# Kernel tuning notes

Measured on AMD Instinct MI355X. Metric: run time of the kernel, lower is better.

## Reference

```python
import jax, jax.numpy as jnp
import numpy as np

N = 50000      # nodes
E = 1600000    # edges (avg degree 32)
F_IN = 128     # num_features
DIM = 64       # hidden dim
L = 3          # num_gc_layers
G = 500        # graphs in batch


def setup_inputs() -> dict:
    key = jax.random.key(0)
    ks = jax.random.split(key, 16)
    inp = {}
    inp["x"] = jax.random.normal(ks[0], (N, F_IN), dtype=jnp.float32)
    inp["edge_index"] = jax.random.randint(ks[1], (2, E), 0, N, dtype=jnp.int32)
    inp["batch"] = jnp.sort(jax.random.randint(ks[2], (N,), 0, G, dtype=jnp.int32))
    # GIN layer MLP params: layer0 maps F_IN->DIM->DIM, later layers DIM->DIM->DIM
    d_in = F_IN
    ki = 3
    for i in range(L):
        inp[f"W1_{i}"] = jax.random.normal(ks[ki], (d_in, DIM), dtype=jnp.float32) / np.sqrt(d_in); ki += 1
        inp[f"b1_{i}"] = jnp.zeros((DIM,), dtype=jnp.float32)
        inp[f"W2_{i}"] = jax.random.normal(ks[ki], (DIM, DIM), dtype=jnp.float32) / np.sqrt(DIM); ki += 1
        inp[f"b2_{i}"] = jnp.zeros((DIM,), dtype=jnp.float32)
        d_in = DIM
    # final scoring head: concat readout -> dim * L inputs, 1 output
    inp["Wm"] = jax.random.normal(ks[ki], (DIM * L, 1), dtype=jnp.float32) / np.sqrt(DIM * L)
    inp["bm"] = jnp.zeros((1,), dtype=jnp.float32)
    return inp


def _segment_softmax(scores, seg, num_segments):
    # numerically stable softmax over elements grouped by seg; scores [M, 1]
    m = jax.ops.segment_max(scores, seg, num_segments=num_segments)
    e = jnp.exp(scores - m[seg])
    denom = jax.ops.segment_sum(e, seg, num_segments=num_segments)
    return e / denom[seg]


def _forward(x, edge_index, batch, params):
    src, dst = edge_index[0], edge_index[1]
    n = x.shape[0]
    xs = []
    h = x
    for i in range(L):
        W1, b1, W2, b2 = params[4 * i: 4 * i + 4]
        # GINConv (eps=0): h_i <- MLP(h_i + sum_{j->i} h_j)
        agg = jax.ops.segment_sum(h[src], dst, num_segments=n)
        h = jax.nn.relu((h + agg) @ W1 + b1) @ W2 + b2
        if i != L - 1:
            h = jax.nn.relu(h)
        xs.append(h)
    node_prob = jnp.concatenate(xs, axis=1)            # concat readout [N, DIM*L]
    Wm, bm = params[4 * L], params[4 * L + 1]
    node_score = node_prob @ Wm + bm                   # [N, 1]
    # lift_node_score_to_edge_score
    src_score = node_score[src]                        # [E, 1]
    dst_score = node_score[dst]
    edge_score = src_score * dst_score
    edge_prop = _segment_softmax(edge_score, dst, n)   # softmax over edges per dst
    new_score = jax.ops.segment_sum(src_score * edge_prop, dst, num_segments=n)
    node_score = node_score + new_score
    # final softmax over nodes grouped by graph id
    return _segment_softmax(node_score, batch, G)


def reference(x, edge_index, batch, W1_0, b1_0, W2_0, b2_0, W1_1, b1_1, W2_1, b2_1,
              W1_2, b1_2, W2_2, b2_2, Wm, bm):
    params = [W1_0, b1_0, W2_0, b2_0, W1_1, b1_1, W2_1, b2_1,
              W1_2, b1_2, W2_2, b2_2, Wm, bm]
    return _forward(x, edge_index, batch, params)
```

## Files before the change

### kernel.cpp

```cpp
#include <hip/hip_runtime.h>
#include <hip/hip_fp16.h>
#include <math.h>

#define N_NODES 50000
#define N_EDGES 1600000
#define N_GRAPH 500
#define CHUNKS 128
#define EPC (N_EDGES / CHUNKS)
#define NP1 (N_NODES + 1)
#define NIT ((EPC + 1023) / 1024)
#define GEMM_BLOCKS 128

__device__ __forceinline__ float rl(float v, int k) {
    return __int_as_float(__builtin_amdgcn_readlane(__float_as_int(v), k));
}
__device__ __forceinline__ void hacc16(float4& A, float4& B, uint4 w) {
    float2 f0 = __half22float2(*reinterpret_cast<__half2*>(&w.x));
    float2 f1 = __half22float2(*reinterpret_cast<__half2*>(&w.y));
    float2 f2 = __half22float2(*reinterpret_cast<__half2*>(&w.z));
    float2 f3 = __half22float2(*reinterpret_cast<__half2*>(&w.w));
    A.x += f0.x; A.y += f0.y; A.z += f1.x; A.w += f1.y;
    B.x += f2.x; B.y += f2.y; B.z += f3.x; B.w += f3.y;
}

__global__ __launch_bounds__(1024) void hist_gemm0_kernel(const int* __restrict__ src,
                                                          const int* __restrict__ dst,
                                                          int* __restrict__ csrc_chunk,
                                                          unsigned short* __restrict__ locs,
                                                          const float* __restrict__ x,
                                                          const float* __restrict__ W1,
                                                          __half* __restrict__ y0, int N) {
    __shared__ unsigned packed[N_NODES / 2];
    __shared__ unsigned aux[1024];
    const int tid = threadIdx.x;

    if (blockIdx.x < CHUNKS) {
        const int c = blockIdx.x;
        const int s0 = c * EPC;

        for (int i = tid; i < N_NODES / 2; i += 1024) packed[i] = 0;
        __syncthreads();

        unsigned short lrv[NIT];
#pragma unroll
        for (int it = 0; it < NIT; it++) {
            int e = s0 + it * 1024 + tid;
            if (e < s0 + EPC) {
                int d = dst[e];
                int sh = (d & 1) * 16;
                unsigned old = atomicAdd(&packed[d >> 1], 1u << sh);
                lrv[it] = (unsigned short)((old >> sh) & 0xffffu);
            }
        }
        __syncthreads();

        const int W = 25;
        int w0 = tid * W;
        int w1 = min(w0 + W, N_NODES / 2);
        unsigned run = 0;
        for (int i = w0; i < w1; i++) {
            unsigned v = packed[i];
            unsigned lo = v & 0xffffu, hi = v >> 16;
            packed[i] = run | ((run + lo) << 16);
            run += lo + hi;
        }
        aux[tid] = run;
        __syncthreads();
        for (int off = 1; off < 1024; off <<= 1) {
            unsigned t = (tid >= off) ? aux[tid - off] : 0;
            __syncthreads();
            aux[tid] += t;
            __syncthreads();
        }
        unsigned b0 = (tid == 0) ? 0 : aux[tid - 1];
        if (b0) {
            unsigned addv = b0 | (b0 << 16);
            for (int i = w0; i < w1; i++) packed[i] += addv;
        }
        __syncthreads();

        int* outc = csrc_chunk + (size_t)c * EPC;
#pragma unroll
        for (int it = 0; it < NIT; it++) {
            int e = s0 + it * 1024 + tid;
            if (e < s0 + EPC) {
                int d = dst[e];
                unsigned pw = packed[d >> 1];
                unsigned loc = (d & 1) ? (pw >> 16) : (pw & 0xffffu);
                outc[loc + lrv[it]] = src[e];
            }
        }
        unsigned short* lc = locs + (size_t)c * NP1;
        for (int d = tid; d <= N_NODES; d += 1024) {
            unsigned short loc;
            if (d == N_NODES) {
                loc = (unsigned short)EPC;
            } else {
                unsigned pw = packed[d >> 1];
                loc = (unsigned short)((d & 1) ? (pw >> 16) : (pw & 0xffffu));
            }
            lc[d] = loc;
        }
    } else {
        float* sW = (float*)packed;
        for (int i = tid; i < 64 * 64; i += 1024) sW[i] = W1[64 * 64 + i];
        __syncthreads();
        int lane = tid & 63;
        float w[64];
#pragma unroll
        for (int k = 0; k < 64; k++) w[k] = W1[k * 64 + lane];
        int wid = ((blockIdx.x - CHUNKS) * 1024 + tid) >> 6;
        const int totalWaves = GEMM_BLOCKS * 16;
        for (int node = wid; node < N; node += totalWaves) {
            float xa = x[(size_t)node * 128 + lane];
            float xb = x[(size_t)node * 128 + 64 + lane];
            float a0 = 0.f, a1 = 0.f, a2 = 0.f, a3 = 0.f;
#pragma unroll
            for (int k = 0; k < 64; k += 4) {
                a0 = fmaf(rl(xa, k + 0), w[k + 0], a0);
                a1 = fmaf(rl(xa, k + 1), w[k + 1], a1);
                a2 = fmaf(rl(xa, k + 2), w[k + 2], a2);
                a3 = fmaf(rl(xa, k + 3), w[k + 3], a3);
            }
#pragma unroll
            for (int k = 0; k < 64; k += 4) {
                a0 = fmaf(rl(xb, k + 0), sW[(k + 0) * 64 + lane], a0);
                a1 = fmaf(rl(xb, k + 1), sW[(k + 1) * 64 + lane], a1);
                a2 = fmaf(rl(xb, k + 2), sW[(k + 2) * 64 + lane], a2);
                a3 = fmaf(rl(xb, k + 3), sW[(k + 3) * 64 + lane], a3);
            }
            y0[(size_t)node * 64 + lane] = __float2half((a0 + a1) + (a2 + a3));
        }
    }
}

__global__ __launch_bounds__(1024) void base_scan1_kernel(const unsigned short* __restrict__ locs,
                                                          unsigned short* __restrict__ base,
                                                          int* __restrict__ deg,
                                                          int* __restrict__ part, int N) {
    int d = blockIdx.x * 1024 + threadIdx.x;
    int run = 0;
    if (d < N) {
#pragma unroll 8
        for (int c = 0; c < CHUNKS; c++) {
            int l0 = locs[(size_t)c * NP1 + d];
            int l1 = locs[(size_t)c * NP1 + d + 1];
            base[(size_t)c * N + d] = (unsigned short)run;
            run += l1 - l0;
        }
        deg[d] = run;
    }
    int v = run;
#pragma unroll
    for (int o = 32; o >= 1; o >>= 1) v += __shfl_xor(v, o);
    __shared__ int red[16];
    if ((threadIdx.x & 63) == 0) red[threadIdx.x >> 6] = v;
    __syncthreads();
    if (threadIdx.x == 0) {
        int s = 0;
#pragma unroll
        for (int k = 0; k < 16; k++) s += red[k];
        part[blockIdx.x] = s;
    }
}

__global__ void scan2_kernel(int* __restrict__ part, int nb) {
    int lane = threadIdx.x;
    int v = (lane < nb) ? part[lane] : 0;
    int orig = v;
#pragma unroll
    for (int o = 1; o < 64; o <<= 1) {
        int t = __shfl_up(v, o);
        if (lane >= o) v += t;
    }
    if (lane < nb) part[lane] = v - orig;
    if (lane == nb - 1) part[nb] = v;
}

__global__ __launch_bounds__(1024) void scan3_kernel(const int* __restrict__ deg,
                                                     const int* __restrict__ part,
                                                     int* __restrict__ rowptr, int N) {
    int i = blockIdx.x * 1024 + threadIdx.x;
    int lane = threadIdx.x & 63;
    int w = threadIdx.x >> 6;
    int v = (i < N) ? deg[i] : 0;
    int inc = v;
#pragma unroll
    for (int o = 1; o < 64; o <<= 1) {
        int t = __shfl_up(inc, o);
        if (lane >= o) inc += t;
    }
    __shared__ int wsum[16];
    if (lane == 63) wsum[w] = inc;
    __syncthreads();
    if (threadIdx.x < 16) {
        int x = wsum[threadIdx.x];
        int xo = x;
#pragma unroll
        for (int o = 1; o < 16; o <<= 1) {
            int t = __shfl_up(x, o);
            if ((int)threadIdx.x >= o) x += t;
        }
        wsum[threadIdx.x] = x - xo;
    }
    __syncthreads();
    int b = part[blockIdx.x] + wsum[w];
    if (i < N) {
        rowptr[i] = b + inc - v;
        if (i == N - 1) rowptr[N] = b + inc;
    }
}

__global__ __launch_bounds__(256) void gatherfill_kernel(const int* __restrict__ csrc_chunk,
                                                         const unsigned short* __restrict__ locs,
                                                         const unsigned short* __restrict__ base,
                                                         const int* __restrict__ rowptr,
                                                         int* __restrict__ csr_src) {
    const int perXcd = N_NODES / 8;
    int xcd = blockIdx.x & 7;
    int idx = (blockIdx.x >> 3) * 4 + (threadIdx.x >> 6);
    if (idx >= perXcd) return;
    int wid = xcd * perXcd + idx;
    int lane = threadIdx.x & 63;
    int rp = rowptr[wid];
#pragma unroll
    for (int cc = 0; cc < 2; cc++) {
        int c = lane + cc * 64;
        const unsigned short* lc = locs + (size_t)c * NP1;
        int l0 = lc[wid];
        int l1 = lc[wid + 1];
        int cnt = l1 - l0;
        int ob = rp + (int)base[(size_t)c * N_NODES + wid];
        const int* in = csrc_chunk + (size_t)c * EPC + l0;
        for (int i = 0; i < cnt; i++) csr_src[ob + i] = in[i];
    }
}

__global__ __launch_bounds__(256) void agg_kernel(const __half* __restrict__ yh,
                                                  const int* __restrict__ rowptr,
                                                  const int* __restrict__ csr_src,
                                                  float* __restrict__ u, int N) {
    int wid = (blockIdx.x * 256 + threadIdx.x) >> 6;
    int lane = threadIdx.x & 63;
    if (wid >= N) return;
    int q = lane >> 3;
    int r = lane & 7;
    int start = rowptr[wid];
    int end = rowptr[wid + 1];
    float4 A = make_float4(0.f, 0.f, 0.f, 0.f);
    float4 B = make_float4(0.f, 0.f, 0.f, 0.f);
    int j = start;
    for (; j + 64 <= end; j += 64) {
        int s0 = csr_src[j + q];
        int s1 = csr_src[j + 8 + q];
        int s2 = csr_src[j + 16 + q];
        int s3 = csr_src[j + 24 + q];
        int s4 = csr_src[j + 32 + q];
        int s5 = csr_src[j + 40 + q];
        int s6 = csr_src[j + 48 + q];
        int s7 = csr_src[j + 56 + q];
        uint4 w0 = *(const uint4*)(yh + (size_t)s0 * 64 + r * 8);
        uint4 w1 = *(const uint4*)(yh + (size_t)s1 * 64 + r * 8);
        uint4 w2 = *(const uint4*)(yh + (size_t)s2 * 64 + r * 8);
        uint4 w3 = *(const uint4*)(yh + (size_t)s3 * 64 + r * 8);
        uint4 w4 = *(const uint4*)(yh + (size_t)s4 * 64 + r * 8);
        uint4 w5 = *(const uint4*)(yh + (size_t)s5 * 64 + r * 8);
        uint4 w6 = *(const uint4*)(yh + (size_t)s6 * 64 + r * 8);
        uint4 w7 = *(const uint4*)(yh + (size_t)s7 * 64 + r * 8);
        hacc16(A, B, w0); hacc16(A, B, w1); hacc16(A, B, w2); hacc16(A, B, w3);
        hacc16(A, B, w4); hacc16(A, B, w5); hacc16(A, B, w6); hacc16(A, B, w7);
    }
#pragma unroll
    for (int m = 0; m < 8; m++) {
        int e = j + 8 * m + q;
        if (e < end) {
            int s = csr_src[e];
            uint4 w = *(const uint4*)(yh + (size_t)s * 64 + r * 8);
            hacc16(A, B, w);
        }
    }
#pragma unroll
    for (int o = 8; o <= 32; o <<= 1) {
        A.x += __shfl_xor(A.x, o); A.y += __shfl_xor(A.y, o);
        A.z += __shfl_xor(A.z, o); A.w += __shfl_xor(A.w, o);
        B.x += __shfl_xor(B.x, o); B.y += __shfl_xor(B.y, o);
        B.z += __shfl_xor(B.z, o); B.w += __shfl_xor(B.w, o);
    }
    if (lane < 8) {
        uint4 w = *(const uint4*)(yh + (size_t)wid * 64 + r * 8);
        hacc16(A, B, w);
        *(float4*)(u + (size_t)wid * 64 + r * 8) = A;
        *(float4*)(u + (size_t)wid * 64 + r * 8 + 4) = B;
    }
}

template <int LAYER>
__global__ __launch_bounds__(256) void mlpAB_kernel(const float* __restrict__ u,
                                                    const float* __restrict__ b1,
                                                    const float* __restrict__ W2,
                                                    const float* __restrict__ b2,
                                                    const float* __restrict__ W1n,
                                                    const float* __restrict__ Wm,
                                                    __half* __restrict__ ynext,
                                                    float* __restrict__ score,
                                                    int N, int totalWaves) {
    int lane = threadIdx.x & 63;
    int wid = (blockIdx.x * 256 + threadIdx.x) >> 6;
    float w2[64], w1[64];
#pragma unroll
    for (int k = 0; k < 64; k++) w2[k] = W2[k * 64 + lane];
#pragma unroll
    for (int k = 0; k < 64; k++) w1[k] = W1n[k * 64 + lane];
    float bb1 = b1[lane], bb2 = b2[lane], wm = Wm[LAYER * 64 + lane];

    int node = wid;
    float uin = (node < N) ? u[(size_t)node * 64 + lane] : 0.f;
    for (; node < N; node += totalWaves) {
        int nn = node + totalWaves;
        float unext = (nn < N) ? u[(size_t)nn * 64 + lane] : 0.f;
        float t = fmaxf(uin + bb1, 0.f);
        float a0 = 0.f, a1 = 0.f, a2 = 0.f, a3 = 0.f;
#pragma unroll
        for (int k = 0; k < 64; k += 4) {
            a0 = fmaf(rl(t, k + 0), w2[k + 0], a0);
            a1 = fmaf(rl(t, k + 1), w2[k + 1], a1);
            a2 = fmaf(rl(t, k + 2), w2[k + 2], a2);
            a3 = fmaf(rl(t, k + 3), w2[k + 3], a3);
        }
        float h = fmaxf(bb2 + ((a0 + a1) + (a2 + a3)), 0.f);
        float p = h * wm;
#pragma unroll
        for (int o = 32; o >= 1; o >>= 1) p += __shfl_xor(p, o);
        if (lane == 0) {
            if (LAYER == 0) score[node] = p;
            else score[node] += p;
        }
        float y0 = 0.f, y1 = 0.f, y2 = 0.f, y3 = 0.f;
#pragma unroll
        for (int k = 0; k < 64; k += 4) {
            y0 = fmaf(rl(h, k + 0), w1[k + 0], y0);
            y1 = fmaf(rl(h, k + 1), w1[k + 1], y1);
            y2 = fmaf(rl(h, k + 2), w1[k + 2], y2);
            y3 = fmaf(rl(h, k + 3), w1[k + 3], y3);
        }
        ynext[(size_t)node * 64 + lane] = __float2half((y0 + y1) + (y2 + y3));
        uin = unext;
    }
}

__global__ __launch_bounds__(256) void mlpA2_kernel(const float* __restrict__ u,
                                                    const float* __restrict__ b1,
                                                    const float* __restrict__ W2,
                                                    const float* __restrict__ b2,
                                                    const float* __restrict__ Wm,
                                                    float* __restrict__ score,
                                                    int N, int totalWaves) {
    int lane = threadIdx.x & 63;
    int wid = (blockIdx.x * 256 + threadIdx.x) >> 6;
    float w2[64];
#pragma unroll
    for (int k = 0; k < 64; k++) w2[k] = W2[k * 64 + lane];
    float bb1 = b1[lane], bb2 = b2[lane], wm = Wm[2 * 64 + lane];

    int node = wid;
    float uin = (node < N) ? u[(size_t)node * 64 + lane] : 0.f;
    for (; node < N; node += totalWaves) {
        int nn = node + totalWaves;
        float unext = (nn < N) ? u[(size_t)nn * 64 + lane] : 0.f;
        float t = fmaxf(uin + bb1, 0.f);
        float a0 = 0.f, a1 = 0.f, a2 = 0.f, a3 = 0.f;
#pragma unroll
        for (int k = 0; k < 64; k += 4) {
            a0 = fmaf(rl(t, k + 0), w2[k + 0], a0);
            a1 = fmaf(rl(t, k + 1), w2[k + 1], a1);
            a2 = fmaf(rl(t, k + 2), w2[k + 2], a2);
            a3 = fmaf(rl(t, k + 3), w2[k + 3], a3);
        }
        float h = bb2 + ((a0 + a1) + (a2 + a3));
        float p = h * wm;
#pragma unroll
        for (int o = 32; o >= 1; o >>= 1) p += __shfl_xor(p, o);
        if (lane == 0) score[node] += p;
        uin = unext;
    }
}

__global__ __launch_bounds__(256) void edge_softmax_kernel(const float* __restrict__ score,
                                                           const int* __restrict__ rowptr,
                                                           const int* __restrict__ csr_src,
                                                           const float* __restrict__ bm,
                                                           float* __restrict__ nsf, int N) {
    int wid = (blockIdx.x * blockDim.x + threadIdx.x) >> 6;
    int lane = threadIdx.x & 63;
    if (wid >= N) return;
    float b = bm[0];
    float sd = score[wid] + b;
    int start = rowptr[wid];
    int end = rowptr[wid + 1];
    bool has0 = (start + lane < end);
    float ss0 = 0.f;
    float m = -INFINITY;
    if (has0) {
        ss0 = score[csr_src[start + lane]] + b;
        m = ss0 * sd;
    }
    for (int j = start + 64 + lane; j < end; j += 64) {
        float ss = score[csr_src[j]] + b;
        m = fmaxf(m, ss * sd);
    }
#pragma unroll
    for (int o = 32; o >= 1; o >>= 1) m = fmaxf(m, __shfl_xor(m, o));
    float se = 0.f, swe = 0.f;
    if (m > -INFINITY) {
        if (has0) {
            float e0 = expf(ss0 * sd - m);
            se += e0;
            swe += ss0 * e0;
        }
        for (int j = start + 64 + lane; j < end; j += 64) {
            float ss = score[csr_src[j]] + b;
            float e = expf(ss * sd - m);
            se += e;
            swe += ss * e;
        }
#pragma unroll
        for (int o = 32; o >= 1; o >>= 1) {
            se += __shfl_xor(se, o);
            swe += __shfl_xor(swe, o);
        }
    }
    float ns = (se > 0.f) ? (swe / se) : 0.f;
    if (lane == 0) nsf[wid] = sd + ns;
}

__global__ __launch_bounds__(256) void graph_softmax_kernel(const float* __restrict__ nsf,
                                                            const int* __restrict__ batch,
                                                            float* __restrict__ out, int N) {
    int g = blockIdx.x;
    int tid = threadIdx.x;
    int lo = 0, hi = N;
    while (lo < hi) { int mid = (lo + hi) >> 1; if (batch[mid] < g) lo = mid + 1; else hi = mid; }
    int s0 = lo;
    hi = N;
    while (lo < hi) { int mid = (lo + hi) >> 1; if (batch[mid] < g + 1) lo = mid + 1; else hi = mid; }
    int s1 = lo;

    __shared__ float red[4];
    __shared__ float bval;
    float m = -INFINITY;
    for (int i = s0 + tid; i < s1; i += 256) m = fmaxf(m, nsf[i]);
#pragma unroll
    for (int o = 32; o >= 1; o >>= 1) m = fmaxf(m, __shfl_xor(m, o));
    if ((tid & 63) == 0) red[tid >> 6] = m;
    __syncthreads();
    if (tid == 0) bval = fmaxf(fmaxf(red[0], red[1]), fmaxf(red[2], red[3]));
    __syncthreads();
    float bmx = bval;
    float s = 0.f;
    for (int i = s0 + tid; i < s1; i += 256) {
        float e = expf(nsf[i] - bmx);
        out[i] = e;
        s += e;
    }
#pragma unroll
    for (int o = 32; o >= 1; o >>= 1) s += __shfl_xor(s, o);
    __syncthreads();
    if ((tid & 63) == 0) red[tid >> 6] = s;
    __syncthreads();
    if (tid == 0) bval = red[0] + red[1] + red[2] + red[3];
    __syncthreads();
    float inv = 1.f / bval;
    for (int i = s0 + tid; i < s1; i += 256) out[i] *= inv;
}

extern "C" void kernel_launch(void* const* d_in, const int* in_sizes, int n_in,
                              void* d_out, int out_size, void* d_ws, size_t ws_size,
                              hipStream_t stream) {
    const int N = N_NODES, E = N_EDGES;

    const float* x = (const float*)d_in[0];
    const int* ei = (const int*)d_in[1];
    const int* batch = (const int*)d_in[2];
    const float* W1a[3] = {(const float*)d_in[3], (const float*)d_in[7], (const float*)d_in[11]};
    const float* b1a[3] = {(const float*)d_in[4], (const float*)d_in[8], (const float*)d_in[12]};
    const float* W2a[3] = {(const float*)d_in[5], (const float*)d_in[9], (const float*)d_in[13]};
    const float* b2a[3] = {(const float*)d_in[6], (const float*)d_in[10], (const float*)d_in[14]};
    const float* Wm = (const float*)d_in[15];
    const float* bm = (const float*)d_in[16];
    float* out = (float*)d_out;

    const int* srcp = ei;
    const int* dstp = ei + E;

    float* ubuf = (float*)d_ws;
    int* csrc_chunk = (int*)ubuf;
    __half* yA = (__half*)(ubuf + (size_t)N * 64);
    __half* yB = yA + (size_t)N * 64;
    float* score = (float*)(yB + (size_t)N * 64);
    float* nsf = score + N;
    int* deg = (int*)(nsf + N);
    int* rowptr = deg + N;
    int* part = rowptr + N + 1;
    int* csr_src = part + 64;
    unsigned short* locs = (unsigned short*)(csr_src + E);
    unsigned short* base = locs + (size_t)CHUNKS * NP1;

    hist_gemm0_kernel<<<CHUNKS + GEMM_BLOCKS, 1024, 0, stream>>>(srcp, dstp, csrc_chunk, locs,
                                                                 x, W1a[0], yA, N);

    const int nbScan = (N + 1023) / 1024;
    base_scan1_kernel<<<nbScan, 1024, 0, stream>>>(locs, base, deg, part, N);
    scan2_kernel<<<1, 64, 0, stream>>>(part, nbScan);
    scan3_kernel<<<nbScan, 1024, 0, stream>>>(deg, part, rowptr, N);

    const int gfBlocks = 8 * ((N / 8 + 3) / 4);
    gatherfill_kernel<<<gfBlocks, 256, 0, stream>>>(csrc_chunk, locs, base, rowptr, csr_src);

    const int gw = 4096;
    int aggBlocks = (N + 3) / 4;

    agg_kernel<<<aggBlocks, 256, 0, stream>>>(yA, rowptr, csr_src, ubuf, N);
    mlpAB_kernel<0><<<1024, 256, 0, stream>>>(ubuf, b1a[0], W2a[0], b2a[0], W1a[1], Wm, yB, score, N, gw);

    agg_kernel<<<aggBlocks, 256, 0, stream>>>(yB, rowptr, csr_src, ubuf, N);
    mlpAB_kernel<1><<<1024, 256, 0, stream>>>(ubuf, b1a[1], W2a[1], b2a[1], W1a[2], Wm, yA, score, N, gw);

    agg_kernel<<<aggBlocks, 256, 0, stream>>>(yA, rowptr, csr_src, ubuf, N);
    mlpA2_kernel<<<1024, 256, 0, stream>>>(ubuf, b1a[2], W2a[2], b2a[2], Wm, score, N, gw);

    edge_softmax_kernel<<<(N + 3) / 4, 256, 0, stream>>>(score, rowptr, csr_src, bm, nsf, N);

    graph_softmax_kernel<<<N_GRAPH, 256, 0, stream>>>(nsf, batch, out, N);
}
```

Baseline: 372.5 us.

## Move layer-0 GEMM into gather-fill kernel and fold scan2 into scan3

The first-layer x@W1 GEMM moves out of the histogram-sort kernel and is co-launched with the CSR gather-fill kernel as extra 256-thread blocks, so it no longer competes with the LDS-heavy sort blocks. The GEMM now keeps the weights in registers and does two passes over the two 64-wide halves of x, writing and then rereading the half-precision output. This adds a second fp16 rounding and an extra read-modify-write of y0. The separate scan2 launch is removed: each scan3 block reduces the per-block partial sums itself, which saves one kernel launch.

```diff
diff --git a/kernel.cpp b/kernel.cpp
--- a/kernel.cpp
+++ b/kernel.cpp
@@ -9,7 +9,7 @@
 #define EPC (N_EDGES / CHUNKS)
 #define NP1 (N_NODES + 1)
 #define NIT ((EPC + 1023) / 1024)
-#define GEMM_BLOCKS 128
+#define GEMM_BLOCKS 1024
 
 __device__ __forceinline__ float rl(float v, int k) {
     return __int_as_float(__builtin_amdgcn_readlane(__float_as_int(v), k));
@@ -23,114 +23,78 @@
     B.x += f2.x; B.y += f2.y; B.z += f3.x; B.w += f3.y;
 }
 
-__global__ __launch_bounds__(1024) void hist_gemm0_kernel(const int* __restrict__ src,
-                                                          const int* __restrict__ dst,
-                                                          int* __restrict__ csrc_chunk,
-                                                          unsigned short* __restrict__ locs,
-                                                          const float* __restrict__ x,
-                                                          const float* __restrict__ W1,
-                                                          __half* __restrict__ y0, int N) {
+__global__ __launch_bounds__(1024) void histsort_kernel(const int* __restrict__ src,
+                                                        const int* __restrict__ dst,
+                                                        int* __restrict__ csrc_chunk,
+                                                        unsigned short* __restrict__ locs) {
     __shared__ unsigned packed[N_NODES / 2];
     __shared__ unsigned aux[1024];
+    const int c = blockIdx.x;
+    const int s0 = c * EPC;
     const int tid = threadIdx.x;
 
-    if (blockIdx.x < CHUNKS) {
-        const int c = blockIdx.x;
-        const int s0 = c * EPC;
-
-        for (int i = tid; i < N_NODES / 2; i += 1024) packed[i] = 0;
+    for (int i = tid; i < N_NODES / 2; i += 1024) packed[i] = 0;
+    __syncthreads();
+
+    unsigned short lrv[NIT];
+#pragma unroll
+    for (int it = 0; it < NIT; it++) {
+        int e = s0 + it * 1024 + tid;
+        if (e < s0 + EPC) {
+            int d = dst[e];
+            int sh = (d & 1) * 16;
+            unsigned old = atomicAdd(&packed[d >> 1], 1u << sh);
+            lrv[it] = (unsigned short)((old >> sh) & 0xffffu);
+        }
+    }
+    __syncthreads();
+
+    const int W = 25;
+    int w0 = tid * W;
+    int w1 = min(w0 + W, N_NODES / 2);
+    unsigned run = 0;
+    for (int i = w0; i < w1; i++) {
+        unsigned v = packed[i];
+        unsigned lo = v & 0xffffu, hi = v >> 16;
+        packed[i] = run | ((run + lo) << 16);
+        run += lo + hi;
+    }
+    aux[tid] = run;
+    __syncthreads();
+    for (int off = 1; off < 1024; off <<= 1) {
+        unsigned t = (tid >= off) ? aux[tid - off] : 0;
         __syncthreads();
-
-        unsigned short lrv[NIT];
-#pragma unroll
-        for (int it = 0; it < NIT; it++) {
-            int e = s0 + it * 1024 + tid;
-            if (e < s0 + EPC) {
-                int d = dst[e];
-                int sh = (d & 1) * 16;
-                unsigned old = atomicAdd(&packed[d >> 1], 1u << sh);
-                lrv[it] = (unsigned short)((old >> sh) & 0xffffu);
-            }
-        }
+        aux[tid] += t;
         __syncthreads();
-
-        const int W = 25;
-        int w0 = tid * W;
-        int w1 = min(w0 + W, N_NODES / 2);
-        unsigned run = 0;
-        for (int i = w0; i < w1; i++) {
-            unsigned v = packed[i];
-            unsigned lo = v & 0xffffu, hi = v >> 16;
-            packed[i] = run | ((run + lo) << 16);
-            run += lo + hi;
-        }
-        aux[tid] = run;
-        __syncthreads();
-        for (int off = 1; off < 1024; off <<= 1) {
-            unsigned t = (tid >= off) ? aux[tid - off] : 0;
-            __syncthreads();
-            aux[tid] += t;
-            __syncthreads();
-        }
-        unsigned b0 = (tid == 0) ? 0 : aux[tid - 1];
-        if (b0) {
-            unsigned addv = b0 | (b0 << 16);
-            for (int i = w0; i < w1; i++) packed[i] += addv;
-        }
-        __syncthreads();
-
-        int* outc = csrc_chunk + (size_t)c * EPC;
-#pragma unroll
-        for (int it = 0; it < NIT; it++) {
-            int e = s0 + it * 1024 + tid;
-            if (e < s0 + EPC) {
-                int d = dst[e];
-                unsigned pw = packed[d >> 1];
-                unsigned loc = (d & 1) ? (pw >> 16) : (pw & 0xffffu);
-                outc[loc + lrv[it]] = src[e];
-            }
-        }
-        unsigned short* lc = locs + (size_t)c * NP1;
-        for (int d = tid; d <= N_NODES; d += 1024) {
-            unsigned short loc;
-            if (d == N_NODES) {
-                loc = (unsigned short)EPC;
-            } else {
-                unsigned pw = packed[d >> 1];
-                loc = (unsigned short)((d & 1) ? (pw >> 16) : (pw & 0xffffu));
-            }
-            lc[d] = loc;
-        }
-    } else {
-        float* sW = (float*)packed;
-        for (int i = tid; i < 64 * 64; i += 1024) sW[i] = W1[64 * 64 + i];
-        __syncthreads();
-        int lane = tid & 63;
-        float w[64];
-#pragma unroll
-        for (int k = 0; k < 64; k++) w[k] = W1[k * 64 + lane];
-        int wid = ((blockIdx.x - CHUNKS) * 1024 + tid) >> 6;
-        const int totalWaves = GEMM_BLOCKS * 16;
-        for (int node = wid; node < N; node += totalWaves) {
-            float xa = x[(size_t)node * 128 + lane];
-            float xb = x[(size_t)node * 128 + 64 + lane];
-            float a0 = 0.f, a1 = 0.f, a2 = 0.f, a3 = 0.f;
-#pragma unroll
-            for (int k = 0; k < 64; k += 4) {
-                a0 = fmaf(rl(xa, k + 0), w[k + 0], a0);
-                a1 = fmaf(rl(xa, k + 1), w[k + 1], a1);
-                a2 = fmaf(rl(xa, k + 2), w[k + 2], a2);
-                a3 = fmaf(rl(xa, k + 3), w[k + 3], a3);
-            }
-#pragma unroll
-            for (int k = 0; k < 64; k += 4) {
-                a0 = fmaf(rl(xb, k + 0), sW[(k + 0) * 64 + lane], a0);
-                a1 = fmaf(rl(xb, k + 1), sW[(k + 1) * 64 + lane], a1);
-                a2 = fmaf(rl(xb, k + 2), sW[(k + 2) * 64 + lane], a2);
-                a3 = fmaf(rl(xb, k + 3), sW[(k + 3) * 64 + lane], a3);
-            }
-            y0[(size_t)node * 64 + lane] = __float2half((a0 + a1) + (a2 + a3));
-        }
+    }
+    unsigned b0 = (tid == 0) ? 0 : aux[tid - 1];
+    if (b0) {
+        unsigned addv = b0 | (b0 << 16);
+        for (int i = w0; i < w1; i++) packed[i] += addv;
+    }
+    __syncthreads();
+
+    int* outc = csrc_chunk + (size_t)c * EPC;
+#pragma unroll
+    for (int it = 0; it < NIT; it++) {
+        int e = s0 + it * 1024 + tid;
+        if (e < s0 + EPC) {
+            int d = dst[e];
+            unsigned pw = packed[d >> 1];
+            unsigned loc = (d & 1) ? (pw >> 16) : (pw & 0xffffu);
+            outc[loc + lrv[it]] = src[e];
+        }
+    }
+    unsigned short* lc = locs + (size_t)c * NP1;
+    for (int d = tid; d <= N_NODES; d += 1024) {
+        unsigned short loc;
+        if (d == N_NODES) {
+            loc = (unsigned short)EPC;
+        } else {
+            unsigned pw = packed[d >> 1];
+            loc = (unsigned short)((d & 1) ? (pw >> 16) : (pw & 0xffffu));
+        }
+        lc[d] = loc;
     }
 }
 
@@ -164,25 +128,20 @@
     }
 }
 
-__global__ void scan2_kernel(int* __restrict__ part, int nb) {
-    int lane = threadIdx.x;
-    int v = (lane < nb) ? part[lane] : 0;
-    int orig = v;
-#pragma unroll
-    for (int o = 1; o < 64; o <<= 1) {
-        int t = __shfl_up(v, o);
-        if (lane >= o) v += t;
-    }
-    if (lane < nb) part[lane] = v - orig;
-    if (lane == nb - 1) part[nb] = v;
-}
-
 __global__ __launch_bounds__(1024) void scan3_kernel(const int* __restrict__ deg,
                                                      const int* __restrict__ part,
-                                                     int* __restrict__ rowptr, int N) {
-    int i = blockIdx.x * 1024 + threadIdx.x;
+                                                     int* __restrict__ rowptr, int N, int nb) {
+    __shared__ int blockOff;
+    __shared__ int wsum[16];
     int lane = threadIdx.x & 63;
     int w = threadIdx.x >> 6;
+    if (threadIdx.x < 64) {
+        int pv = (lane < nb && lane < (int)blockIdx.x) ? part[lane] : 0;
+#pragma unroll
+        for (int o = 32; o >= 1; o >>= 1) pv += __shfl_xor(pv, o);
+        if (lane == 0) blockOff = pv;
+    }
+    int i = blockIdx.x * 1024 + threadIdx.x;
     int v = (i < N) ? deg[i] : 0;
     int inc = v;
 #pragma unroll
@@ -190,7 +149,6 @@
         int t = __shfl_up(inc, o);
         if (lane >= o) inc += t;
     }
-    __shared__ int wsum[16];
     if (lane == 63) wsum[w] = inc;
     __syncthreads();
     if (threadIdx.x < 16) {
@@ -204,35 +162,75 @@
         wsum[threadIdx.x] = x - xo;
     }
     __syncthreads();
-    int b = part[blockIdx.x] + wsum[w];
+    int b = blockOff + wsum[w];
     if (i < N) {
         rowptr[i] = b + inc - v;
         if (i == N - 1) rowptr[N] = b + inc;
     }
 }
 
-__global__ __launch_bounds__(256) void gatherfill_kernel(const int* __restrict__ csrc_chunk,
-                                                         const unsigned short* __restrict__ locs,
-                                                         const unsigned short* __restrict__ base,
-                                                         const int* __restrict__ rowptr,
-                                                         int* __restrict__ csr_src) {
-    const int perXcd = N_NODES / 8;
-    int xcd = blockIdx.x & 7;
-    int idx = (blockIdx.x >> 3) * 4 + (threadIdx.x >> 6);
-    if (idx >= perXcd) return;
-    int wid = xcd * perXcd + idx;
-    int lane = threadIdx.x & 63;
-    int rp = rowptr[wid];
-#pragma unroll
-    for (int cc = 0; cc < 2; cc++) {
-        int c = lane + cc * 64;
-        const unsigned short* lc = locs + (size_t)c * NP1;
-        int l0 = lc[wid];
-        int l1 = lc[wid + 1];
-        int cnt = l1 - l0;
-        int ob = rp + (int)base[(size_t)c * N_NODES + wid];
-        const int* in = csrc_chunk + (size_t)c * EPC + l0;
-        for (int i = 0; i < cnt; i++) csr_src[ob + i] = in[i];
+__global__ __launch_bounds__(256) void gf_gemm0_kernel(const int* __restrict__ csrc_chunk,
+                                                       const unsigned short* __restrict__ locs,
+                                                       const unsigned short* __restrict__ base,
+                                                       const int* __restrict__ rowptr,
+                                                       int* __restrict__ csr_src,
+                                                       const float* __restrict__ x,
+                                                       const float* __restrict__ W1,
+                                                       __half* __restrict__ y0,
+                                                       int gfBlocks, int N) {
+    if ((int)blockIdx.x < gfBlocks) {
+        const int perXcd = N_NODES / 8;
+        int xcd = blockIdx.x & 7;
+        int idx = (blockIdx.x >> 3) * 4 + (threadIdx.x >> 6);
+        if (idx >= perXcd) return;
+        int wid = xcd * perXcd + idx;
+        int lane = threadIdx.x & 63;
+        int rp = rowptr[wid];
+#pragma unroll
+        for (int cc = 0; cc < 2; cc++) {
+            int c = lane + cc * 64;
+            const unsigned short* lc = locs + (size_t)c * NP1;
+            int l0 = lc[wid];
+            int l1 = lc[wid + 1];
+            int cnt = l1 - l0;
+            int ob = rp + (int)base[(size_t)c * N_NODES + wid];
+            const int* in = csrc_chunk + (size_t)c * EPC + l0;
+            for (int i = 0; i < cnt; i++) csr_src[ob + i] = in[i];
+        }
+    } else {
+        int lane = threadIdx.x & 63;
+        int wid = (((int)blockIdx.x - gfBlocks) * 256 + threadIdx.x) >> 6;
+        const int totalWaves = GEMM_BLOCKS * 4;
+        float w[64];
+#pragma unroll
+        for (int k = 0; k < 64; k++) w[k] = W1[k * 64 + lane];
+        for (int node = wid; node < N; node += totalWaves) {
+            float xa = x[(size_t)node * 128 + lane];
+            float a0 = 0.f, a1 = 0.f, a2 = 0.f, a3 = 0.f;
+#pragma unroll
+            for (int k = 0; k < 64; k += 4) {
+                a0 = fmaf(rl(xa, k + 0), w[k + 0], a0);
+                a1 = fmaf(rl(xa, k + 1), w[k + 1], a1);
+                a2 = fmaf(rl(xa, k + 2), w[k + 2], a2);
+                a3 = fmaf(rl(xa, k + 3), w[k + 3], a3);
+            }
+            y0[(size_t)node * 64 + lane] = __float2half((a0 + a1) + (a2 + a3));
+        }
+#pragma unroll
+        for (int k = 0; k < 64; k++) w[k] = W1[(64 + k) * 64 + lane];
+        for (int node = wid; node < N; node += totalWaves) {
+            float xb = x[(size_t)node * 128 + 64 + lane];
+            float a0 = 0.f, a1 = 0.f, a2 = 0.f, a3 = 0.f;
+#pragma unroll
+            for (int k = 0; k < 64; k += 4) {
+                a0 = fmaf(rl(xb, k + 0), w[k + 0], a0);
+                a1 = fmaf(rl(xb, k + 1), w[k + 1], a1);
+                a2 = fmaf(rl(xb, k + 2), w[k + 2], a2);
+                a3 = fmaf(rl(xb, k + 3), w[k + 3], a3);
+            }
+            float prev = __half2float(y0[(size_t)node * 64 + lane]);
+            y0[(size_t)node * 64 + lane] = __float2half(prev + ((a0 + a1) + (a2 + a3)));
+        }
     }
 }
 
@@ -505,16 +503,15 @@
     unsigned short* locs = (unsigned short*)(csr_src + E);
     unsigned short* base = locs + (size_t)CHUNKS * NP1;
 
-    hist_gemm0_kernel<<<CHUNKS + GEMM_BLOCKS, 1024, 0, stream>>>(srcp, dstp, csrc_chunk, locs,
-                                                                 x, W1a[0], yA, N);
+    histsort_kernel<<<CHUNKS, 1024, 0, stream>>>(srcp, dstp, csrc_chunk, locs);
 
     const int nbScan = (N + 1023) / 1024;
     base_scan1_kernel<<<nbScan, 1024, 0, stream>>>(locs, base, deg, part, N);
-    scan2_kernel<<<1, 64, 0, stream>>>(part, nbScan);
-    scan3_kernel<<<nbScan, 1024, 0, stream>>>(deg, part, rowptr, N);
+    scan3_kernel<<<nbScan, 1024, 0, stream>>>(deg, part, rowptr, N, nbScan);
 
     const int gfBlocks = 8 * ((N / 8 + 3) / 4);
-    gatherfill_kernel<<<gfBlocks, 256, 0, stream>>>(csrc_chunk, locs, base, rowptr, csr_src);
+    gf_gemm0_kernel<<<gfBlocks + GEMM_BLOCKS, 256, 0, stream>>>(csrc_chunk, locs, base, rowptr,
+                                                                csr_src, x, W1a[0], yA, gfBlocks, N);
 
     const int gw = 4096;
     int aggBlocks = (N + 3) / 4;
```

Measured after the change: 356.9 us. 4.2% less time.
